# Optimization experiments

Measured on AMD Instinct MI355X. Metric: run time of the kernel, lower is better.

## Reference

```python
import jax, jax.numpy as jnp
import numpy as np

DIM = 512
H = 8
HS = DIM // H
SCALES = [25, 12, 7]
ATTN_SCALE = HS ** -0.5
EPS = 1e-5


def _ln(x, g, b):
    m = jnp.mean(x, axis=-1, keepdims=True)
    v = jnp.mean((x - m) ** 2, axis=-1, keepdims=True)
    return (x - m) * jax.lax.rsqrt(v + EPS) * g + b


def setup_inputs() -> dict:
    key = jax.random.key(0)
    ks = jax.random.split(key, 12)
    B, T, J, C = 64, 64, 25, DIM
    w = lambda k, s: jax.random.normal(k, s, dtype=jnp.float32) * 0.02
    return {
        "src": jax.random.normal(ks[0], (B, T, J, C), dtype=jnp.float32),
        "spatial_relation": jax.random.normal(ks[1], (B, T, J, J, 2), dtype=jnp.float32),
        "ln1_g": jnp.ones((C,), jnp.float32),
        "ln1_b": jnp.zeros((C,), jnp.float32),
        "Wq": w(ks[2], (3, C, C)),
        "Wk": w(ks[3], (3, C, C)),
        "Wv": w(ks[4], (3, C, C)),
        "pool0_fc1_w": w(ks[5], (C, 2 * C)),
        "pool0_fc1_b": jnp.zeros((2 * C,), jnp.float32),
        "pool0_fc2_w": w(ks[6], (2 * C, SCALES[1])),
        "pool0_fc2_b": jnp.zeros((SCALES[1],), jnp.float32),
        "pool1_fc1_w": w(ks[7], (C, 2 * C)),
        "pool1_fc1_b": jnp.zeros((2 * C,), jnp.float32),
        "pool1_fc2_w": w(ks[8], (2 * C, SCALES[2])),
        "pool1_fc2_b": jnp.zeros((SCALES[2],), jnp.float32),
    }


def reference(src, spatial_relation, ln1_g, ln1_b, Wq, Wk, Wv,
              pool0_fc1_w, pool0_fc1_b, pool0_fc2_w, pool0_fc2_b,
              pool1_fc1_w, pool1_fc1_b, pool1_fc2_w, pool1_fc2_b):
    # NOTE: in the original torch module, the relation-bias terms (R_qk, R_conv,
    # attn_R_qurt) and spatial_relation_emb are computed but never added to the
    # attention logits, so they do not affect the output; faithful output math below.
    B, T, J, C = src.shape
    x = src.reshape(B * T, J, C)
    g_feat = x  # global (query) features, stay at J nodes
    l_feat = x  # local (key/value) features, get pooled
    pools = [
        (pool0_fc1_w, pool0_fc1_b, pool0_fc2_w, pool0_fc2_b),
        (pool1_fc1_w, pool1_fc1_b, pool1_fc2_w, pool1_fc2_b),
    ]
    outs = []
    for i in range(len(SCALES)):
        qn = _ln(g_feat, ln1_g, ln1_b)
        kn = _ln(l_feat, ln1_g, ln1_b)
        q = (qn @ Wq[i]).reshape(B * T, J, H, HS)
        k = (kn @ Wk[i]).reshape(B * T, -1, H, HS)
        v = (kn @ Wv[i]).reshape(B * T, -1, H, HS)
        logits = jnp.einsum('bnhd,bmhd->bhnm', q, k) * ATTN_SCALE
        a = jax.nn.softmax(logits, axis=-1)
        o = jnp.einsum('bhnm,bmhd->bnhd', a, v).reshape(B * T, J, C)
        outs.append(g_feat + o)
        if i < len(SCALES) - 1:
            f1w, f1b, f2w, f2b = pools[i]
            h = jax.nn.gelu(l_feat @ f1w + f1b, approximate=False)
            S = jax.nn.softmax(h @ f2w + f2b, axis=-1)  # (BT, Ni, Ni+1)
            l_feat = jnp.einsum('bns,bnc->bsc', S, l_feat)
    return jnp.mean(jnp.stack(outs, axis=-1), axis=-1)
```

## Files before the change

kernel.cpp:

```cpp
#include <hip/hip_runtime.h>

typedef unsigned short u16;
typedef unsigned int   u32;
typedef _Float16 f16;
typedef __attribute__((ext_vector_type(8))) unsigned short u16x8;
typedef __attribute__((ext_vector_type(8))) _Float16 f16x8;
typedef __attribute__((ext_vector_type(2))) _Float16 f16x2;
typedef __attribute__((ext_vector_type(4))) float f32x4;

__device__ __forceinline__ u16 f2h(float f) {
  f16 h = (f16)f;
  return __builtin_bit_cast(u16, h);
}
__device__ __forceinline__ float h2f(u16 u) {
  return (float)__builtin_bit_cast(f16, u);
}

__global__ __launch_bounds__(256) void prep_w(const float* __restrict__ Wq,
    const float* __restrict__ Wk, const float* __restrict__ Wv,
    const float* __restrict__ f0, const float* __restrict__ f1,
    u16* __restrict__ wt) {
  int t = blockIdx.x * 256 + threadIdx.x;
  float v;
  if (t < 786432) {
    int i = t >> 18, r = t & 262143, n = r >> 9, k = r & 511;
    v = Wq[(size_t)(i << 18) + k * 512 + n];
  } else if (t < 2359296) {
    int r = t - 786432, i = r >> 19, r2 = r & 524287;
    int n = (r2 >> 9) & 511, k = r2 & 511;
    v = ((r2 >> 18) ? Wv : Wk)[(size_t)(i << 18) + k * 512 + n];
  } else if (t < 2883584) {
    int r = t - 2359296, n = r >> 9, k = r & 511;
    v = f0[(size_t)k * 1024 + n];
  } else {
    int r = t - 2883584, n = r >> 9, k = r & 511;
    v = f1[(size_t)k * 1024 + n];
  }
  wt[t] = f2h(v);
}

__global__ __launch_bounds__(256) void ln_f32(const float* __restrict__ x,
    const float* __restrict__ g, const float* __restrict__ bta,
    u16* __restrict__ xn, u16* __restrict__ xb) {
  int row = (blockIdx.x << 2) + (threadIdx.x >> 6);
  int lane = threadIdx.x & 63;
  const float* xr = x + (size_t)row * 512 + (lane << 3);
  float4 a = *(const float4*)xr;
  float4 c = *(const float4*)(xr + 4);
  float v[8] = {a.x, a.y, a.z, a.w, c.x, c.y, c.z, c.w};
  float s = 0.f, s2 = 0.f;
#pragma unroll
  for (int j = 0; j < 8; ++j) { s += v[j]; s2 += v[j] * v[j]; }
  for (int off = 32; off; off >>= 1) { s += __shfl_xor(s, off); s2 += __shfl_xor(s2, off); }
  float mean = s * (1.f / 512.f);
  float var = s2 * (1.f / 512.f) - mean * mean;
  float rs = rsqrtf(var + 1e-5f);
  const float* gp = g + (lane << 3);
  const float* bp = bta + (lane << 3);
  u16x8 pb, pn;
#pragma unroll
  for (int j = 0; j < 8; ++j) {
    pb[j] = f2h(v[j]);
    pn[j] = f2h((v[j] - mean) * rs * gp[j] + bp[j]);
  }
  *(u16x8*)(xb + (size_t)row * 512 + (lane << 3)) = pb;
  *(u16x8*)(xn + (size_t)row * 512 + (lane << 3)) = pn;
}

__global__ __launch_bounds__(256) void ln_b16(const u16* __restrict__ xin,
    const float* __restrict__ g, const float* __restrict__ bta,
    u16* __restrict__ xout) {
  int row = (blockIdx.x << 2) + (threadIdx.x >> 6);
  int lane = threadIdx.x & 63;
  f16x8 u = *(const f16x8*)(xin + (size_t)row * 512 + (lane << 3));
  float v[8];
#pragma unroll
  for (int j = 0; j < 8; ++j) v[j] = (float)u[j];
  float s = 0.f, s2 = 0.f;
#pragma unroll
  for (int j = 0; j < 8; ++j) { s += v[j]; s2 += v[j] * v[j]; }
  for (int off = 32; off; off >>= 1) { s += __shfl_xor(s, off); s2 += __shfl_xor(s2, off); }
  float mean = s * (1.f / 512.f);
  float var = s2 * (1.f / 512.f) - mean * mean;
  float rs = rsqrtf(var + 1e-5f);
  const float* gp = g + (lane << 3);
  const float* bp = bta + (lane << 3);
  u16x8 pn;
#pragma unroll
  for (int j = 0; j < 8; ++j) pn[j] = f2h((v[j] - mean) * rs * gp[j] + bp[j]);
  *(u16x8*)(xout + (size_t)row * 512 + (lane << 3)) = pn;
}

template <bool GELU>
__global__ __launch_bounds__(512, 2) void gemm_bt(const u16* __restrict__ A,
    const u16* __restrict__ Bt, u16* __restrict__ C,
    const float* __restrict__ bias, int M, int N) {
  __shared__ __align__(16) char smem[69632];
  u16* As = (u16*)smem;
  u16* Bs = (u16*)(smem + 32768);
  u16* Cs = (u16*)smem;
  constexpr int LDC = 136;
  int tid = threadIdx.x;
  int w = tid >> 6, lane = tid & 63;
  int nwg = gridDim.x * gridDim.y;
  int wg = blockIdx.x + gridDim.x * blockIdx.y;
  int swz = (wg & 7) * (nwg >> 3) + (wg >> 3);
  int m0 = (swz / gridDim.x) << 8, n0 = (swz % gridDim.x) << 7;
  int wm = (w >> 1) << 6, wn = (w & 1) << 6;
  f32x4 acc[4][4] = {};
  const int grow = tid >> 3;
  const int gcol = (((tid & 7) ^ (grow & 7)) << 3);
  for (int kt = 0; kt < 8; ++kt) {
    __syncthreads();
#pragma unroll
    for (int s = 0; s < 4; ++s) {
      const u16* gA = A + (size_t)(m0 + grow + (s << 6)) * 512 + (kt << 6) + gcol;
      __builtin_amdgcn_global_load_lds(
          (const __attribute__((address_space(1))) u32*)gA,
          (__attribute__((address_space(3))) u32*)(As + tid * 8 + (s << 12)), 16, 0, 0);
    }
#pragma unroll
    for (int s = 0; s < 2; ++s) {
      const u16* gB = Bt + (size_t)(n0 + grow + (s << 6)) * 512 + (kt << 6) + gcol;
      __builtin_amdgcn_global_load_lds(
          (const __attribute__((address_space(1))) u32*)gB,
          (__attribute__((address_space(3))) u32*)(Bs + tid * 8 + (s << 12)), 16, 0, 0);
    }
    asm volatile("s_waitcnt vmcnt(0)" ::: "memory");
    __syncthreads();
#pragma unroll
    for (int kk = 0; kk < 2; ++kk) {
      int slot_w = (kk << 2) + (lane >> 4);
      f16x8 af[4], bfr[4];
#pragma unroll
      for (int mi = 0; mi < 4; ++mi) {
        int rr = wm + (mi << 4) + (lane & 15);
        af[mi] = *(const f16x8*)(As + rr * 64 + ((slot_w ^ (rr & 7)) << 3));
      }
#pragma unroll
      for (int ni = 0; ni < 4; ++ni) {
        int rr = wn + (ni << 4) + (lane & 15);
        bfr[ni] = *(const f16x8*)(Bs + rr * 64 + ((slot_w ^ (rr & 7)) << 3));
      }
#pragma unroll
      for (int mi = 0; mi < 4; ++mi)
#pragma unroll
        for (int ni = 0; ni < 4; ++ni)
          acc[mi][ni] = __builtin_amdgcn_mfma_f32_16x16x32_f16(af[mi], bfr[ni], acc[mi][ni], 0, 0, 0);
    }
  }
  __syncthreads();
  int cr = (lane >> 4) << 2, cc = lane & 15;
#pragma unroll
  for (int mi = 0; mi < 4; ++mi) {
#pragma unroll
    for (int ni = 0; ni < 4; ++ni) {
      float bv = 0.f;
      if (GELU) bv = bias[n0 + wn + (ni << 4) + cc];
#pragma unroll
      for (int j = 0; j < 4; ++j) {
        float v = acc[mi][ni][j];
        if (GELU) { v += bv; v = 0.5f * v * (1.f + erff(v * 0.70710678118f)); }
        Cs[(wm + (mi << 4) + cr + j) * LDC + wn + (ni << 4) + cc] = f2h(v);
      }
    }
  }
  __syncthreads();
  int r = tid >> 1, hc = (tid & 1) << 6;
  u16* crow = C + (size_t)(m0 + r) * N + n0 + hc;
  const u16* srow = Cs + r * LDC + hc;
#pragma unroll
  for (int i = 0; i < 8; ++i)
    *(u16x8*)(crow + (i << 3)) = *(const u16x8*)(srow + (i << 3));
}

template <int NKV, int PMODE, int MINW>
__global__ __launch_bounds__(512, MINW) void attn(const u16* __restrict__ Q,
    const u16* __restrict__ KV, const u16* __restrict__ xb,
    float* __restrict__ out, u16* __restrict__ p) {
  constexpr int G = 8;
  constexpr int ELEMS = NKV * 1024;
  __shared__ __align__(16) u16 KVl[2][ELEMS];
  int tid = threadIdx.x;
  int b0 = blockIdx.x * G;
  int h = tid >> 6, r = tid & 63, n = r >> 1, half = r & 1;
  int dbase = (h << 6) + (half << 5);
  bool act = (n < 25);
  f16x8 q8[4];
  if (act) {
    const u16* qr = Q + (size_t)(b0 * 25 + n) * 512 + dbase;
#pragma unroll
    for (int i = 0; i < 4; ++i) q8[i] = *(const f16x8*)(qr + (i << 3));
  }
  __builtin_amdgcn_sched_barrier(0);
  {
    const u16* src = KV + (size_t)b0 * ELEMS;
    for (int e = tid * 8; e < ELEMS; e += 4096)
      __builtin_amdgcn_global_load_lds(
          (const __attribute__((address_space(1))) u32*)(src + e),
          (__attribute__((address_space(3))) u32*)(KVl[0] + e), 16, 0, 0);
  }
  asm volatile("s_waitcnt vmcnt(0)" ::: "memory");
  __syncthreads();
  for (int t = 0; t < G; ++t) {
    const u16* KVc = KVl[t & 1];
    int b = b0 + t;
    size_t rowoff = (size_t)(b * 25 + n) * 512 + dbase;
    f16x8 pv16[4];
    f16x8 xv16[4];
    float4 ov[8];
    if (act) {
      if (PMODE == 3 || PMODE == 4) {
        const u16* prow = p + rowoff;
#pragma unroll
        for (int i = 0; i < 4; ++i) pv16[i] = *(const f16x8*)(prow + (i << 3));
      }
      if (PMODE == 0 || PMODE == 4) {
        const u16* xrow = xb + rowoff;
#pragma unroll
        for (int i = 0; i < 4; ++i) xv16[i] = *(const f16x8*)(xrow + (i << 3));
      }
      if (PMODE == 1) {
        const float* orow = out + rowoff;
#pragma unroll
        for (int i = 0; i < 8; ++i) ov[i] = *(const float4*)(orow + (i << 2));
      }
    }
    f16x8 qn[4];
    if (act && t + 1 < G) {
      const u16* qr = Q + (size_t)((b + 1) * 25 + n) * 512 + dbase;
#pragma unroll
      for (int i = 0; i < 4; ++i) qn[i] = *(const f16x8*)(qr + (i << 3));
    }
    __builtin_amdgcn_sched_barrier(0);
    if (t + 1 < G) {
      const u16* src = KV + (size_t)(b + 1) * ELEMS;
      u16* dst = KVl[(t + 1) & 1];
      for (int e = tid * 8; e < ELEMS; e += 4096)
        __builtin_amdgcn_global_load_lds(
            (const __attribute__((address_space(1))) u32*)(src + e),
            (__attribute__((address_space(3))) u32*)(dst + e), 16, 0, 0);
    }
    if (act) {
      const f16x2* q2 = (const f16x2*)q8;
      float s[NKV];
      float mx = -1e30f;
#pragma unroll
      for (int m = 0; m < NKV; ++m) {
        const u16* kr = KVc + m * 1024 + dbase;
        f16x2 a0 = {(f16)0.f, (f16)0.f}, a1 = a0;
#pragma unroll
        for (int i = 0; i < 4; ++i) {
          f16x8 kv = *(const f16x8*)(kr + (i << 3));
          const f16x2* k2 = (const f16x2*)&kv;
          a0 += q2[i * 4 + 0] * k2[0];
          a1 += q2[i * 4 + 1] * k2[1];
          a0 += q2[i * 4 + 2] * k2[2];
          a1 += q2[i * 4 + 3] * k2[3];
        }
        f16x2 at = a0 + a1;
        float d = (float)at[0] + (float)at[1];
        d += __shfl_xor(d, 1);
        s[m] = d * 0.125f;
        mx = fmaxf(mx, s[m]);
      }
      float sum = 0.f;
#pragma unroll
      for (int m = 0; m < NKV; ++m) { s[m] = __expf(s[m] - mx); sum += s[m]; }
      f16x8 o8[4] = {};
#pragma unroll
      for (int m = 0; m < NKV; ++m) {
        f16 ah = (f16)s[m];
        f16x8 av = {ah, ah, ah, ah, ah, ah, ah, ah};
        const u16* vr = KVc + m * 1024 + 512 + dbase;
#pragma unroll
        for (int i = 0; i < 4; ++i) {
          f16x8 vv = *(const f16x8*)(vr + (i << 3));
          o8[i] += vv * av;
        }
      }
      if (PMODE == 0 || PMODE == 1) {
        float sc = (1.f / sum) * (1.f / 3.f);
        float* orow = out + rowoff;
#pragma unroll
        for (int i = 0; i < 4; ++i) {
#pragma unroll
          for (int j = 0; j < 8; j += 4) {
            float4 rr;
            if (PMODE == 0) {
              rr.x = (float)o8[i][j + 0] * sc + (float)xv16[i][j + 0];
              rr.y = (float)o8[i][j + 1] * sc + (float)xv16[i][j + 1];
              rr.z = (float)o8[i][j + 2] * sc + (float)xv16[i][j + 2];
              rr.w = (float)o8[i][j + 3] * sc + (float)xv16[i][j + 3];
            } else {
              float4 pv = ov[i * 2 + (j >> 2)];
              rr.x = (float)o8[i][j + 0] * sc + pv.x;
              rr.y = (float)o8[i][j + 1] * sc + pv.y;
              rr.z = (float)o8[i][j + 2] * sc + pv.z;
              rr.w = (float)o8[i][j + 3] * sc + pv.w;
            }
            *(float4*)(orow + (i << 3) + j) = rr;
          }
        }
      } else if (PMODE == 2 || PMODE == 3) {
        float sc = 1.f / sum;
        u16* prow = p + rowoff;
#pragma unroll
        for (int i = 0; i < 4; ++i) {
          u16x8 pk;
#pragma unroll
          for (int j = 0; j < 8; ++j) {
            float v = (float)o8[i][j] * sc;
            if (PMODE == 3) v += (float)pv16[i][j];
            pk[j] = f2h(v);
          }
          *(u16x8*)(prow + (i << 3)) = pk;
        }
      } else {
        float sc = 1.f / sum;
        float* orow = out + rowoff;
#pragma unroll
        for (int i = 0; i < 4; ++i) {
#pragma unroll
          for (int j = 0; j < 8; j += 4) {
            float4 rr;
            rr.x = (float)xv16[i][j + 0] + ((float)pv16[i][j + 0] + (float)o8[i][j + 0] * sc) * (1.f / 3.f);
            rr.y = (float)xv16[i][j + 1] + ((float)pv16[i][j + 1] + (float)o8[i][j + 1] * sc) * (1.f / 3.f);
            rr.z = (float)xv16[i][j + 2] + ((float)pv16[i][j + 2] + (float)o8[i][j + 2] * sc) * (1.f / 3.f);
            rr.w = (float)xv16[i][j + 3] + ((float)pv16[i][j + 3] + (float)o8[i][j + 3] * sc) * (1.f / 3.f);
            *(float4*)(orow + (i << 3) + j) = rr;
          }
        }
      }
    }
    asm volatile("s_waitcnt vmcnt(0)" ::: "memory");
    __syncthreads();
#pragma unroll
    for (int i = 0; i < 4; ++i) q8[i] = qn[i];
  }
}

template <int NIN, int NOUT>
__global__ __launch_bounds__(256) void pool(const u16* __restrict__ h,
    const u16* __restrict__ lf, const float* __restrict__ w2,
    const float* __restrict__ b2, u16* __restrict__ lout) {
  __shared__ __align__(16) float W2l[1024 * NOUT];
  __shared__ __align__(16) u16 Xl[NIN * 512];
  __shared__ __align__(16) float Sl[NIN * NOUT];
  int b = blockIdx.x, tid = threadIdx.x;
  for (int e = tid; e < 1024 * NOUT; e += 256) W2l[e] = w2[e];
  for (int e = tid * 8; e < NIN * 512; e += 2048)
    *(u16x8*)(Xl + e) = *(const u16x8*)(lf + (size_t)b * NIN * 512 + e);
  __syncthreads();
  if (tid < NIN * 8) {
    int nn = tid >> 3, sub = tid & 7;
    float pl[NOUT] = {};
    const u16* hr = h + (size_t)(b * NIN + nn) * 1024;
    for (int cc = 0; cc < 128; ++cc) {
      int c = sub + (cc << 3);
      float hv = h2f(hr[c]);
#pragma unroll
      for (int s2 = 0; s2 < NOUT; ++s2) pl[s2] += hv * W2l[c * NOUT + s2];
    }
#pragma unroll
    for (int s2 = 0; s2 < NOUT; ++s2) {
      pl[s2] += __shfl_down(pl[s2], 4, 8);
      pl[s2] += __shfl_down(pl[s2], 2, 8);
      pl[s2] += __shfl_down(pl[s2], 1, 8);
    }
    if (sub == 0) {
      float mx = -1e30f;
#pragma unroll
      for (int s2 = 0; s2 < NOUT; ++s2) { pl[s2] += b2[s2]; mx = fmaxf(mx, pl[s2]); }
      float sum = 0.f;
#pragma unroll
      for (int s2 = 0; s2 < NOUT; ++s2) { pl[s2] = __expf(pl[s2] - mx); sum += pl[s2]; }
      float inv = 1.f / sum;
#pragma unroll
      for (int s2 = 0; s2 < NOUT; ++s2) Sl[nn * NOUT + s2] = pl[s2] * inv;
    }
  }
  __syncthreads();
  int c0 = tid << 1;
#pragma unroll
  for (int s2 = 0; s2 < NOUT; ++s2) {
    float a0 = 0.f, a1 = 0.f;
#pragma unroll
    for (int nn = 0; nn < NIN; ++nn) {
      float wv = Sl[nn * NOUT + s2];
      a0 += wv * h2f(Xl[nn * 512 + c0]);
      a1 += wv * h2f(Xl[nn * 512 + c0 + 1]);
    }
    u32 pk = (u32)f2h(a0) | ((u32)f2h(a1) << 16);
    *(u32*)(lout + (size_t)(b * NOUT + s2) * 512 + c0) = pk;
  }
}

extern "C" void kernel_launch(void* const* d_in, const int* in_sizes, int n_in,
                              void* d_out, int out_size, void* d_ws, size_t ws_size,
                              hipStream_t stream) {
  const float* src = (const float*)d_in[0];
  const float* g    = (const float*)d_in[2];
  const float* bt   = (const float*)d_in[3];
  const float* Wq   = (const float*)d_in[4];
  const float* Wk   = (const float*)d_in[5];
  const float* Wv   = (const float*)d_in[6];
  const float* f0w  = (const float*)d_in[7];
  const float* f0b  = (const float*)d_in[8];
  const float* f0w2 = (const float*)d_in[9];
  const float* f0b2 = (const float*)d_in[10];
  const float* f1w  = (const float*)d_in[11];
  const float* f1b  = (const float*)d_in[12];
  const float* f1w2 = (const float*)d_in[13];
  const float* f1b2 = (const float*)d_in[14];
  float* out = (float*)d_out;
  char* ws = (char*)d_ws;

  u16* wt  = (u16*)(ws + 0);
  u16* xn  = (u16*)(ws + 6815744);
  u16* xb  = (u16*)(ws + 111673344);
  u16* qb  = (u16*)(ws + 216530944);
  u16* B1  = (u16*)(ws + 321388544);
  u16* l1  = (u16*)(ws + 426246144);
  u16* kn1 = (u16*)(ws + 476577792);
  u16* l2  = qb;
  u16* kn2 = qb + 14680064;
  bool bigws = ws_size >= 640000000ull;
  u16* pbuf = (u16*)(ws + 526909440);

  prep_w<<<13312, 256, 0, stream>>>(Wq, Wk, Wv, f0w, f1w, wt);
  ln_f32<<<25600, 256, 0, stream>>>(src, g, bt, xn, xb);

  gemm_bt<false><<<dim3(4, 400), 512, 0, stream>>>(xn, wt, qb, nullptr, 102400, 512);
  for (int s = 0; s < 2; ++s) {
    size_t ro = (size_t)s * 51200;
    gemm_bt<false><<<dim3(8, 200), 512, 0, stream>>>(xn + ro * 512, wt + 786432, B1, nullptr, 51200, 1024);
    if (bigws)
      attn<25, 2, 1><<<256, 512, 0, stream>>>(qb + ro * 512, B1, xb + ro * 512, out + ro * 512, pbuf + ro * 512);
    else
      attn<25, 0, 1><<<256, 512, 0, stream>>>(qb + ro * 512, B1, xb + ro * 512, out + ro * 512, pbuf);
  }

  for (int s = 0; s < 2; ++s) {
    size_t ro = (size_t)s * 51200;
    gemm_bt<true><<<dim3(8, 200), 512, 0, stream>>>(xb + ro * 512, wt + 2359296, B1, f0b, 51200, 1024);
    pool<25, 12><<<2048, 256, 0, stream>>>(B1, xb + ro * 512, f0w2, f0b2, l1 + (size_t)s * 2048 * 12 * 512);
  }
  ln_b16<<<12288, 256, 0, stream>>>(l1, g, bt, kn1);

  gemm_bt<false><<<dim3(4, 400), 512, 0, stream>>>(xn, wt + 262144, qb, nullptr, 102400, 512);
  gemm_bt<false><<<dim3(8, 192), 512, 0, stream>>>(kn1, wt + 786432 + 524288, B1, nullptr, 49152, 1024);
  if (bigws)
    attn<12, 3, 2><<<512, 512, 0, stream>>>(qb, B1, xb, out, pbuf);
  else
    attn<12, 1, 2><<<512, 512, 0, stream>>>(qb, B1, xb, out, pbuf);

  gemm_bt<true><<<dim3(8, 192), 512, 0, stream>>>(l1, wt + 2883584, B1, f1b, 49152, 1024);
  pool<12, 7><<<4096, 256, 0, stream>>>(B1, l1, f1w2, f1b2, l2);
  ln_b16<<<7168, 256, 0, stream>>>(l2, g, bt, kn2);

  gemm_bt<false><<<dim3(8, 112), 512, 0, stream>>>(kn2, wt + 786432 + 1048576, B1, nullptr, 28672, 1024);
  gemm_bt<false><<<dim3(4, 400), 512, 0, stream>>>(xn, wt + 524288, qb, nullptr, 102400, 512);
  if (bigws)
    attn<7, 4, 2><<<512, 512, 0, stream>>>(qb, B1, xb, out, pbuf);
  else
    attn<7, 1, 2><<<512, 512, 0, stream>>>(qb, B1, xb, out, pbuf);
}
```

Measured before the change: 1.738 ms.

## Double-buffer GEMM LDS tiles and shrink workgroup tile to 128x128

The shared-memory GEMM now uses two LDS buffers. The global-to-LDS loads for the next K-step are issued before the MFMAs on the current step, so load latency overlaps compute instead of stalling each iteration. The workgroup tile shrinks from 256x128 with 512 threads to 128x128 with 256 threads, which doubles the grid size for every GEMM launch. In exchange there is less A-tile reuse per workgroup, more global traffic for B, and LDS use of 64KB per block that may limit occupancy.

```diff
diff --git a/kernel.cpp b/kernel.cpp
--- a/kernel.cpp
+++ b/kernel.cpp
@@ -92,12 +92,10 @@
 }
 
 template <bool GELU>
-__global__ __launch_bounds__(512, 2) void gemm_bt(const u16* __restrict__ A,
+__global__ __launch_bounds__(256, 2) void gemm_bt(const u16* __restrict__ A,
     const u16* __restrict__ Bt, u16* __restrict__ C,
     const float* __restrict__ bias, int M, int N) {
-  __shared__ __align__(16) char smem[69632];
-  u16* As = (u16*)smem;
-  u16* Bs = (u16*)(smem + 32768);
+  __shared__ __align__(16) char smem[65536];
   u16* Cs = (u16*)smem;
   constexpr int LDC = 136;
   int tid = threadIdx.x;
@@ -105,29 +103,38 @@
   int nwg = gridDim.x * gridDim.y;
   int wg = blockIdx.x + gridDim.x * blockIdx.y;
   int swz = (wg & 7) * (nwg >> 3) + (wg >> 3);
-  int m0 = (swz / gridDim.x) << 8, n0 = (swz % gridDim.x) << 7;
-  int wm = (w >> 1) << 6, wn = (w & 1) << 6;
+  int m0 = (swz / gridDim.x) << 7, n0 = (swz % gridDim.x) << 7;
+  int wm = (w & 1) << 6, wn = (w >> 1) << 6;
   f32x4 acc[4][4] = {};
   const int grow = tid >> 3;
   const int gcol = (((tid & 7) ^ (grow & 7)) << 3);
+#define GSTAGE(kt, bi)                                                          \
+  {                                                                             \
+    u16* dA = (u16*)(smem + ((bi) << 14));                                      \
+    u16* dB = (u16*)(smem + 32768 + ((bi) << 14));                              \
+    _Pragma("unroll")                                                           \
+    for (int s = 0; s < 4; ++s) {                                               \
+      const u16* gA = A + (size_t)(m0 + grow + (s << 5)) * 512 + ((kt) << 6) + gcol; \
+      __builtin_amdgcn_global_load_lds(                                         \
+          (const __attribute__((address_space(1))) u32*)gA,                     \
+          (__attribute__((address_space(3))) u32*)(dA + tid * 8 + (s << 11)), 16, 0, 0); \
+    }                                                                           \
+    _Pragma("unroll")                                                           \
+    for (int s = 0; s < 4; ++s) {                                               \
+      const u16* gB = Bt + (size_t)(n0 + grow + (s << 5)) * 512 + ((kt) << 6) + gcol; \
+      __builtin_amdgcn_global_load_lds(                                         \
+          (const __attribute__((address_space(1))) u32*)gB,                     \
+          (__attribute__((address_space(3))) u32*)(dB + tid * 8 + (s << 11)), 16, 0, 0); \
+    }                                                                           \
+  }
+  GSTAGE(0, 0);
+  asm volatile("s_waitcnt vmcnt(0)" ::: "memory");
+  __syncthreads();
+  int cur = 0;
   for (int kt = 0; kt < 8; ++kt) {
-    __syncthreads();
-#pragma unroll
-    for (int s = 0; s < 4; ++s) {
-      const u16* gA = A + (size_t)(m0 + grow + (s << 6)) * 512 + (kt << 6) + gcol;
-      __builtin_amdgcn_global_load_lds(
-          (const __attribute__((address_space(1))) u32*)gA,
-          (__attribute__((address_space(3))) u32*)(As + tid * 8 + (s << 12)), 16, 0, 0);
-    }
-#pragma unroll
-    for (int s = 0; s < 2; ++s) {
-      const u16* gB = Bt + (size_t)(n0 + grow + (s << 6)) * 512 + (kt << 6) + gcol;
-      __builtin_amdgcn_global_load_lds(
-          (const __attribute__((address_space(1))) u32*)gB,
-          (__attribute__((address_space(3))) u32*)(Bs + tid * 8 + (s << 12)), 16, 0, 0);
-    }
-    asm volatile("s_waitcnt vmcnt(0)" ::: "memory");
-    __syncthreads();
+    if (kt + 1 < 8) GSTAGE(kt + 1, cur ^ 1);
+    const u16* As = (const u16*)(smem + (cur << 14));
+    const u16* Bs = (const u16*)(smem + 32768 + (cur << 14));
 #pragma unroll
     for (int kk = 0; kk < 2; ++kk) {
       int slot_w = (kk << 2) + (lane >> 4);
@@ -148,8 +155,11 @@
         for (int ni = 0; ni < 4; ++ni)
           acc[mi][ni] = __builtin_amdgcn_mfma_f32_16x16x32_f16(af[mi], bfr[ni], acc[mi][ni], 0, 0, 0);
     }
-  }
-  __syncthreads();
+    asm volatile("s_waitcnt vmcnt(0)" ::: "memory");
+    __syncthreads();
+    cur ^= 1;
+  }
+#undef GSTAGE
   int cr = (lane >> 4) << 2, cc = lane & 15;
 #pragma unroll
   for (int mi = 0; mi < 4; ++mi) {
@@ -431,10 +441,10 @@
   prep_w<<<13312, 256, 0, stream>>>(Wq, Wk, Wv, f0w, f1w, wt);
   ln_f32<<<25600, 256, 0, stream>>>(src, g, bt, xn, xb);
 
-  gemm_bt<false><<<dim3(4, 400), 512, 0, stream>>>(xn, wt, qb, nullptr, 102400, 512);
+  gemm_bt<false><<<dim3(4, 800), 256, 0, stream>>>(xn, wt, qb, nullptr, 102400, 512);
   for (int s = 0; s < 2; ++s) {
     size_t ro = (size_t)s * 51200;
-    gemm_bt<false><<<dim3(8, 200), 512, 0, stream>>>(xn + ro * 512, wt + 786432, B1, nullptr, 51200, 1024);
+    gemm_bt<false><<<dim3(8, 400), 256, 0, stream>>>(xn + ro * 512, wt + 786432, B1, nullptr, 51200, 1024);
     if (bigws)
       attn<25, 2, 1><<<256, 512, 0, stream>>>(qb + ro * 512, B1, xb + ro * 512, out + ro * 512, pbuf + ro * 512);
     else
@@ -443,24 +453,24 @@
 
   for (int s = 0; s < 2; ++s) {
     size_t ro = (size_t)s * 51200;
-    gemm_bt<true><<<dim3(8, 200), 512, 0, stream>>>(xb + ro * 512, wt + 2359296, B1, f0b, 51200, 1024);
+    gemm_bt<true><<<dim3(8, 400), 256, 0, stream>>>(xb + ro * 512, wt + 2359296, B1, f0b, 51200, 1024);
     pool<25, 12><<<2048, 256, 0, stream>>>(B1, xb + ro * 512, f0w2, f0b2, l1 + (size_t)s * 2048 * 12 * 512);
   }
   ln_b16<<<12288, 256, 0, stream>>>(l1, g, bt, kn1);
 
-  gemm_bt<false><<<dim3(4, 400), 512, 0, stream>>>(xn, wt + 262144, qb, nullptr, 102400, 512);
-  gemm_bt<false><<<dim3(8, 192), 512, 0, stream>>>(kn1, wt + 786432 + 524288, B1, nullptr, 49152, 1024);
+  gemm_bt<false><<<dim3(4, 800), 256, 0, stream>>>(xn, wt + 262144, qb, nullptr, 102400, 512);
+  gemm_bt<false><<<dim3(8, 384), 256, 0, stream>>>(kn1, wt + 786432 + 524288, B1, nullptr, 49152, 1024);
   if (bigws)
     attn<12, 3, 2><<<512, 512, 0, stream>>>(qb, B1, xb, out, pbuf);
   else
     attn<12, 1, 2><<<512, 512, 0, stream>>>(qb, B1, xb, out, pbuf);
 
-  gemm_bt<true><<<dim3(8, 192), 512, 0, stream>>>(l1, wt + 2883584, B1, f1b, 49152, 1024);
+  gemm_bt<true><<<dim3(8, 384), 256, 0, stream>>>(l1, wt + 2883584, B1, f1b, 49152, 1024);
   pool<12, 7><<<4096, 256, 0, stream>>>(B1, l1, f1w2, f1b2, l2);
   ln_b16<<<7168, 256, 0, stream>>>(l2, g, bt, kn2);
 
-  gemm_bt<false><<<dim3(8, 112), 512, 0, stream>>>(kn2, wt + 786432 + 1048576, B1, nullptr, 28672, 1024);
-  gemm_bt<false><<<dim3(4, 400), 512, 0, stream>>>(xn, wt + 524288, qb, nullptr, 102400, 512);
+  gemm_bt<false><<<dim3(8, 224), 256, 0, stream>>>(kn2, wt + 786432 + 1048576, B1, nullptr, 28672, 1024);
+  gemm_bt<false><<<dim3(4, 800), 256, 0, stream>>>(xn, wt + 524288, qb, nullptr, 102400, 512);
   if (bigws)
     attn<7, 4, 2><<<512, 512, 0, stream>>>(qb, B1, xb, out, pbuf);
   else
```

New measurement: 1.788 ms. 2.9% more time.

## Triple-buffer GEMM K-loop with async global-to-LDS prefetch two stages ahead

Applied to the files above, without the earlier changes.

Replaces the single-buffered load-wait-compute loop in gemm_bt with a three-stage LDS ring that issues global_load_lds for tile kt+2 while computing tile kt, using partial vmcnt waits. This is meant to hide global memory latency behind MFMA work. LDS grows to 144KB, so occupancy drops from two workgroups per CU to one (launch bounds changed to 512,1), which could offset the gain.

```diff
diff --git a/kernel.cpp b/kernel.cpp
--- a/kernel.cpp
+++ b/kernel.cpp
@@ -92,12 +92,10 @@
 }
 
 template <bool GELU>
-__global__ __launch_bounds__(512, 2) void gemm_bt(const u16* __restrict__ A,
+__global__ __launch_bounds__(512, 1) void gemm_bt(const u16* __restrict__ A,
     const u16* __restrict__ Bt, u16* __restrict__ C,
     const float* __restrict__ bias, int M, int N) {
-  __shared__ __align__(16) char smem[69632];
-  u16* As = (u16*)smem;
-  u16* Bs = (u16*)(smem + 32768);
+  __shared__ __align__(16) char smem[147456];
   u16* Cs = (u16*)smem;
   constexpr int LDC = 136;
   int tid = threadIdx.x;
@@ -110,24 +108,37 @@
   f32x4 acc[4][4] = {};
   const int grow = tid >> 3;
   const int gcol = (((tid & 7) ^ (grow & 7)) << 3);
+#define GSTAGE(kt, bi)                                                          \
+  {                                                                             \
+    u16* dA = (u16*)(smem + (bi) * 49152);                                      \
+    u16* dB = (u16*)(smem + (bi) * 49152 + 32768);                              \
+    _Pragma("unroll")                                                           \
+    for (int s = 0; s < 4; ++s) {                                               \
+      const u16* gA = A + (size_t)(m0 + grow + (s << 6)) * 512 + ((kt) << 6) + gcol; \
+      __builtin_amdgcn_global_load_lds(                                         \
+          (const __attribute__((address_space(1))) u32*)gA,                     \
+          (__attribute__((address_space(3))) u32*)(dA + tid * 8 + (s << 12)), 16, 0, 0); \
+    }                                                                           \
+    _Pragma("unroll")                                                           \
+    for (int s = 0; s < 2; ++s) {                                               \
+      const u16* gB = Bt + (size_t)(n0 + grow + (s << 6)) * 512 + ((kt) << 6) + gcol; \
+      __builtin_amdgcn_global_load_lds(                                         \
+          (const __attribute__((address_space(1))) u32*)gB,                     \
+          (__attribute__((address_space(3))) u32*)(dB + tid * 8 + (s << 12)), 16, 0, 0); \
+    }                                                                           \
+  }
+  GSTAGE(0, 0);
+  GSTAGE(1, 1);
   for (int kt = 0; kt < 8; ++kt) {
+    if (kt < 7) { asm volatile("s_waitcnt vmcnt(6)" ::: "memory"); }
+    else        { asm volatile("s_waitcnt vmcnt(0)" ::: "memory"); }
     __syncthreads();
-#pragma unroll
-    for (int s = 0; s < 4; ++s) {
-      const u16* gA = A + (size_t)(m0 + grow + (s << 6)) * 512 + (kt << 6) + gcol;
-      __builtin_amdgcn_global_load_lds(
-          (const __attribute__((address_space(1))) u32*)gA,
-          (__attribute__((address_space(3))) u32*)(As + tid * 8 + (s << 12)), 16, 0, 0);
-    }
-#pragma unroll
-    for (int s = 0; s < 2; ++s) {
-      const u16* gB = Bt + (size_t)(n0 + grow + (s << 6)) * 512 + (kt << 6) + gcol;
-      __builtin_amdgcn_global_load_lds(
-          (const __attribute__((address_space(1))) u32*)gB,
-          (__attribute__((address_space(3))) u32*)(Bs + tid * 8 + (s << 12)), 16, 0, 0);
-    }
-    asm volatile("s_waitcnt vmcnt(0)" ::: "memory");
-    __syncthreads();
+    if (kt + 2 < 8) {
+      int bi = (kt + 2) % 3;
+      GSTAGE(kt + 2, bi);
+    }
+    const u16* As = (const u16*)(smem + (kt % 3) * 49152);
+    const u16* Bs = (const u16*)(smem + (kt % 3) * 49152 + 32768);
 #pragma unroll
     for (int kk = 0; kk < 2; ++kk) {
       int slot_w = (kk << 2) + (lane >> 4);
@@ -149,6 +160,7 @@
           acc[mi][ni] = __builtin_amdgcn_mfma_f32_16x16x32_f16(af[mi], bfr[ni], acc[mi][ni], 0, 0, 0);
     }
   }
+#undef GSTAGE
   __syncthreads();
   int cr = (lane >> 4) << 2, cc = lane & 15;
 #pragma unroll
```

Result: slower. 1.946 ms (+12.0%).
